# Optimization experiments

Measured on AMD Instinct MI355X. Metric: run time of the kernel, lower is better.

## Reference

```python
import jax, jax.numpy as jnp
import numpy as np

NUM_ORI = 4
VM_R, VM_RG = 10.0, 15.0
B_INH, G_INH = 1.5, 1.0
VM_W, VM_W2 = 0.1, 0.4
VM_WG, VM_W2G = 0.2, 0.4
BORDER_K = 11   # int(10*1.1)=11, already odd
GROUP_K = 23    # int(15*1.5)=22 -> +1 to make odd


def create_von_mises(size, r0, theta0, centered, w, w2):
    x = np.arange(size) - size / 2
    y = -(np.arange(size) - size / 2)
    X, Y = np.meshgrid(x, y)
    if centered:
        X = X + r0 * np.cos(theta0)
        Y = Y + r0 * np.sin(theta0)
    r = np.sqrt(X ** 2 + Y ** 2)
    th = np.arctan2(Y, X)
    # np.i0 == scipy.special.iv(0, .) for real args (I0 is even)
    return np.exp(r0 * w * np.cos(th - theta0)) / np.i0(w2 * (r - r0))


def make_filters():
    borders, groups = [], []
    for ori in np.arange(0.0, 180.0, 180.0 / NUM_ORI):
        a = ori * np.pi / 180.0
        b = (ori + 180.0) * np.pi / 180.0
        borders.append(create_von_mises(BORDER_K, VM_R, a, True, VM_W, VM_W2))
        borders.append(create_von_mises(BORDER_K, VM_R, b, True, VM_W, VM_W2))
        g1 = create_von_mises(GROUP_K, VM_RG, a, False, VM_W, VM_W2)
        g2 = create_von_mises(GROUP_K, VM_RG, b, False, VM_WG, VM_W2G)
        groups += [g1, g1, g2, g2]
    # only border filters are normalized to [-1, 1] in the original code
    borders = [f / (f.max() / 2.0) - 1.0 for f in borders]
    Wb = np.stack(borders)[:, None].astype(np.float32)   # [2*O, 1, 11, 11]
    Wg = np.stack(groups)[:, None].astype(np.float32)    # [4*O, 1, 23, 23]
    return jnp.asarray(Wb), jnp.asarray(Wg)


def setup_inputs() -> dict:
    key = jax.random.key(0)
    inp = jax.random.uniform(key, (4, 2, 512, 512), dtype=jnp.float32)
    Wb, Wg = make_filters()
    return {"inp": inp, "W_border": Wb, "W_group": Wg}


def _conv(x, w, pad, groups):
    return jax.lax.conv_general_dilated(
        x, w, (1, 1), [(pad, pad), (pad, pad)],
        dimension_numbers=("NCHW", "OIHW", "NCHW"),
        feature_group_count=groups)


def _spike(v):
    # LIF with tau_mem=0.01, zero initial v_mem, single step: alpha=exp(-1/tau)~0,
    # so v_mem = input; spike when v_mem >= threshold (1.0).
    return (v >= 1.0).astype(v.dtype)


def reference(inp, W_border, W_group):
    B, _, H, W = inp.shape
    pad_b = (BORDER_K - 1) // 2
    pad_g = (GROUP_K - 1) // 2
    # border ownership: conv each polarity with the 8 von-Mises filters + LIF
    pos = _spike(_conv(inp[:, 0:1], W_border, pad_b, 1))  # [B, 2*O, H, W]
    neg = _spike(_conv(inp[:, 1:2], W_border, pad_b, 1))
    vmap_ = inp.sum(1)[:, None]                           # [B, 1, H, W]
    pe, po = pos[:, 0::2], pos[:, 1::2]   # even=ori, odd=opposite ori
    ne, no = neg[:, 0::2], neg[:, 1::2]
    b13 = _spike(vmap_ * (pe - no * B_INH)) + _spike(vmap_ * (ne - po * B_INH))
    b24 = _spike(vmap_ * (po - ne * B_INH)) + _spike(vmap_ * (no - pe * B_INH))
    # winner-take-all over orientations
    diff = b13 - b24                                      # [B, O, H, W]
    tp = jnp.abs(diff)
    wta = jax.lax.stop_gradient(
        (tp == tp.max(axis=1, keepdims=True)).astype(inp.dtype))
    b1p = _spike(wta * diff)
    b1n = _spike(-(wta * diff))
    # channel order is ori-major: [t1_o, t2_o, t3_o, t4_o] per orientation
    border = jnp.stack(
        [b1p * b13, b1p * b24 * G_INH, b1n * b24, b1n * b13 * G_INH],
        axis=2).reshape(B, 4 * NUM_ORI, H, W)
    g = _spike(_conv(border, W_group, pad_g, 4 * NUM_ORI))
    g = g.reshape(B, NUM_ORI, 4, H, W)
    return (_spike(g[:, :, 0] - g[:, :, 1])
            + _spike(g[:, :, 2] - g[:, :, 3])).sum(1)     # [B, H, W]
```

## Files before the change

kernel.cpp:

```cpp
#include <hip/hip_runtime.h>

#define HH 512
#define WW 512
#define NB 4

typedef float v2f __attribute__((ext_vector_type(2)));

#define K1 11
#define PAD1 5
#define T1X 32
#define T1Y 32
#define IN1 42
#define S1B 44

__global__ __launch_bounds__(256, 4) void stage1_kernel(
    const float* __restrict__ inp, const float* __restrict__ Wb,
    unsigned char* __restrict__ border)
{
    __shared__ __align__(16) float s0[IN1 * S1B];
    __shared__ __align__(16) float s1[IN1 * S1B];

    const int b   = blockIdx.z;
    const int tx0 = blockIdx.x * T1X;
    const int ty0 = blockIdx.y * T1Y;
    const float* in0 = inp + ((size_t)b * 2 + 0) * (HH * WW);
    const float* in1 = inp + ((size_t)b * 2 + 1) * (HH * WW);

    for (int i = threadIdx.x; i < IN1 * IN1; i += 256) {
        int iy = i / IN1, ix = i - iy * IN1;
        int gy = ty0 + iy - PAD1, gx = tx0 + ix - PAD1;
        bool ok = (gy >= 0) & (gy < HH) & (gx >= 0) & (gx < WW);
        int idx = gy * WW + gx;
        s0[iy * S1B + ix] = ok ? in0[idx] : 0.f;
        s1[iy * S1B + ix] = ok ? in1[idx] : 0.f;
    }
    __syncthreads();

    const int lx  = threadIdx.x & 7;
    const int ly  = threadIdx.x >> 3;
    const int px0 = lx * 4;
    const int py  = ly;

    float accP[8][4], accN[8][4];
    #pragma unroll
    for (int c = 0; c < 8; c++)
        #pragma unroll
        for (int p = 0; p < 4; p++) { accP[c][p] = 0.f; accN[c][p] = 0.f; }

    #pragma unroll 1
    for (int ky = 0; ky < K1; ky++) {
        float a0[14], a1[14];
        const float2* r0 = (const float2*)&s0[(py + ky) * S1B + px0];
        const float2* r1 = (const float2*)&s1[(py + ky) * S1B + px0];
        #pragma unroll
        for (int r = 0; r < 7; r++) {
            *(float2*)&a0[2 * r] = r0[r];
            *(float2*)&a1[2 * r] = r1[r];
        }
        #pragma unroll
        for (int c = 0; c < 8; c++) {
            #pragma unroll
            for (int kx = 0; kx < K1; kx++) {
                const float wv = Wb[c * 121 + ky * 11 + kx];
                #pragma unroll
                for (int p = 0; p < 4; p++) {
                    accP[c][p] = fmaf(a0[kx + p], wv, accP[c][p]);
                    accN[c][p] = fmaf(a1[kx + p], wv, accN[c][p]);
                }
            }
        }
    }

    const int gy  = ty0 + py;
    const int gxb = tx0 + px0;

    float vm[4];
    #pragma unroll
    for (int p = 0; p < 4; p++)
        vm[p] = s0[(py + PAD1) * S1B + px0 + PAD1 + p]
              + s1[(py + PAD1) * S1B + px0 + PAD1 + p];

    float b13[4][4], b24[4][4];
    #pragma unroll
    for (int o = 0; o < 4; o++) {
        #pragma unroll
        for (int p = 0; p < 4; p++) {
            float pe = (accP[2 * o    ][p] >= 1.f) ? 1.f : 0.f;
            float po = (accP[2 * o + 1][p] >= 1.f) ? 1.f : 0.f;
            float ne = (accN[2 * o    ][p] >= 1.f) ? 1.f : 0.f;
            float no = (accN[2 * o + 1][p] >= 1.f) ? 1.f : 0.f;
            float sa = (vm[p] * (pe - 1.5f * no) >= 1.f) ? 1.f : 0.f;
            float sb = (vm[p] * (ne - 1.5f * po) >= 1.f) ? 1.f : 0.f;
            b13[o][p] = sa + sb;
            float sc = (vm[p] * (po - 1.5f * ne) >= 1.f) ? 1.f : 0.f;
            float sd = (vm[p] * (no - 1.5f * pe) >= 1.f) ? 1.f : 0.f;
            b24[o][p] = sc + sd;
        }
    }
    float mxp[4];
    #pragma unroll
    for (int p = 0; p < 4; p++) {
        float m = 0.f;
        #pragma unroll
        for (int o = 0; o < 4; o++) m = fmaxf(m, fabsf(b13[o][p] - b24[o][p]));
        mxp[p] = m;
    }
    #pragma unroll
    for (int o = 0; o < 4; o++) {
        unsigned w0 = 0, w1 = 0, w2 = 0, w3 = 0;
        #pragma unroll
        for (int p = 0; p < 4; p++) {
            float d   = b13[o][p] - b24[o][p];
            float wta = (fabsf(d) == mxp[p]) ? 1.f : 0.f;
            float b1p = (wta * d >= 1.f)    ? 1.f : 0.f;
            float b1n = (-(wta * d) >= 1.f) ? 1.f : 0.f;
            w0 |= (unsigned)(unsigned char)(b1p * b13[o][p]) << (8 * p);
            w1 |= (unsigned)(unsigned char)(b1p * b24[o][p]) << (8 * p);
            w2 |= (unsigned)(unsigned char)(b1n * b24[o][p]) << (8 * p);
            w3 |= (unsigned)(unsigned char)(b1n * b13[o][p]) << (8 * p);
        }
        size_t base = (((size_t)b * 16 + 4 * o) * HH + gy) * WW + gxb;
        *(unsigned*)&border[base]                       = w0;
        *(unsigned*)&border[base + (size_t)HH * WW]     = w1;
        *(unsigned*)&border[base + (size_t)2 * HH * WW] = w2;
        *(unsigned*)&border[base + (size_t)3 * HH * WW] = w3;
    }
}

#define K2 23
#define PAD2 11
#define T2X 32
#define T2Y 256
#define SROW 18
#define R2 278

__device__ __forceinline__ float ubyte_f(unsigned dw, int byi) {
    return (float)((dw >> (8 * byi)) & 0xffu);
}

__device__ __forceinline__ void s2_load(const unsigned* __restrict__ tile,
                                        int trow, int lx, unsigned d[8])
{
    const uint2* tp2 = (const uint2*)&tile[trow * SROW + 2 * lx];
    #pragma unroll
    for (int r2 = 0; r2 < 4; r2++) {
        uint2 v = tp2[r2];
        d[2 * r2] = v.x; d[2 * r2 + 1] = v.y;
    }
}

__global__ __launch_bounds__(256, 4) void stage2_kernel(
    const unsigned char* __restrict__ border, const float* __restrict__ Wg,
    unsigned char* __restrict__ gsp)
{
    __shared__ unsigned tile[R2 * SROW];

    const int z   = blockIdx.z;
    const int b   = z >> 4;
    const int c   = z & 15;
    const int tx0 = blockIdx.x * T2X;
    const int ty0 = blockIdx.y * T2Y;
    const unsigned char* bp = border + ((size_t)b * 16 + c) * (HH * WW);

    for (int i = threadIdx.x; i < R2 * 16; i += 256) {
        int iy = i >> 4, cc = i & 15;
        int gy  = ty0 - PAD2 + iy;
        int gx0 = tx0 - 12 + 4 * cc;
        unsigned u = 0;
        if (((unsigned)gy < HH) & ((unsigned)gx0 < WW))
            u = *(const unsigned*)(bp + (size_t)gy * WW + gx0);
        tile[iy * SROW + cc] = u;
    }
    __syncthreads();

    const int lx = threadIdx.x & 3;
    const int ly = threadIdx.x >> 2;
    const int px = lx * 8;
    const int py = ly * 4;

    v2f acc2[4][4];
    #pragma unroll
    for (int dy = 0; dy < 4; dy++)
        #pragma unroll
        for (int i = 0; i < 4; i++) acc2[dy][i] = (v2f){0.f, 0.f};

    const float* wc = Wg + c * (K2 * K2);

    unsigned dc[8];
    s2_load(tile, py + 0, lx, dc);

    #pragma unroll 1
    for (int t = 0; t < 26; t++) {
        v2f aE[15], aO[15];
        #pragma unroll
        for (int e = 0; e < 15; e++)
            aE[e] = (v2f){ubyte_f(dc[(2*e)   >> 2], (2*e)   & 3),
                          ubyte_f(dc[(2*e+1) >> 2], (2*e+1) & 3)};
        #pragma unroll
        for (int o = 0; o < 15; o++)
            aO[o] = (v2f){ubyte_f(dc[(2*o+1) >> 2], (2*o+1) & 3),
                          ubyte_f(dc[(2*o+2) >> 2], (2*o+2) & 3)};
        if (t < 25) s2_load(tile, py + t + 1, lx, dc);

        #pragma unroll
        for (int dy = 0; dy < 4; dy++) {
            const int ky = t - dy;
            if (ky >= 0 && ky < K2) {
                const float* wr = wc + ky * K2;
                #pragma unroll
                for (int kx = 0; kx < K2; kx++) {
                    const float wv = wr[kx];
                    const v2f wb = (v2f){wv, wv};
                    #pragma unroll
                    for (int i = 0; i < 4; i++) {
                        const v2f op = (kx & 1) ? aE[i + (kx + 1) / 2]
                                                : aO[i + kx / 2];
                        acc2[dy][i] = __builtin_elementwise_fma(op, wb, acc2[dy][i]);
                    }
                }
            }
        }
    }

    const int ox = tx0 + px;
    unsigned char* gp = gsp + ((size_t)b * 16 + c) * (HH * WW);
    #pragma unroll
    for (int dy = 0; dy < 4; dy++) {
        const int oy = ty0 + py + dy;
        unsigned lo = 0, hi = 0;
        #pragma unroll
        for (int i = 0; i < 2; i++) {
            lo |= (acc2[dy][i].x >= 1.f ? 1u : 0u) << (16 * i);
            lo |= (acc2[dy][i].y >= 1.f ? 1u : 0u) << (16 * i + 8);
        }
        #pragma unroll
        for (int i = 0; i < 2; i++) {
            hi |= (acc2[dy][i + 2].x >= 1.f ? 1u : 0u) << (16 * i);
            hi |= (acc2[dy][i + 2].y >= 1.f ? 1u : 0u) << (16 * i + 8);
        }
        uint2 v; v.x = lo; v.y = hi;
        *(uint2*)&gp[(size_t)oy * WW + ox] = v;
    }
}

__global__ __launch_bounds__(256) void combine_kernel(
    const unsigned char* __restrict__ gsp, float* __restrict__ out)
{
    const int idx = blockIdx.x * 256 + threadIdx.x;
    const int b = idx >> 16;
    const int r = idx & 65535;
    const unsigned* g = (const unsigned*)gsp;
    const int pb = b * 16;
    unsigned s = 0;
    #pragma unroll
    for (int o = 0; o < 4; o++) {
        unsigned g0 = g[(size_t)(pb + 4 * o + 0) * 65536 + r];
        unsigned g1 = g[(size_t)(pb + 4 * o + 1) * 65536 + r];
        unsigned g2 = g[(size_t)(pb + 4 * o + 2) * 65536 + r];
        unsigned g3 = g[(size_t)(pb + 4 * o + 3) * 65536 + r];
        s += ((g0 & ~g1) & 0x01010101u) + ((g2 & ~g3) & 0x01010101u);
    }
    float4 f;
    f.x = (float)(s & 255u);
    f.y = (float)((s >> 8) & 255u);
    f.z = (float)((s >> 16) & 255u);
    f.w = (float)(s >> 24);
    ((float4*)out)[idx] = f;
}

extern "C" void kernel_launch(void* const* d_in, const int* in_sizes, int n_in,
                              void* d_out, int out_size, void* d_ws, size_t ws_size,
                              hipStream_t stream)
{
    const float* inp = (const float*)d_in[0];
    const float* Wb  = (const float*)d_in[1];
    const float* Wg  = (const float*)d_in[2];
    unsigned char* border = (unsigned char*)d_ws;
    unsigned char* gsp    = border + (size_t)NB * 16 * HH * WW;
    float* out = (float*)d_out;

    dim3 blk(256);
    dim3 g1(WW / T1X, HH / T1Y, NB);
    stage1_kernel<<<g1, blk, 0, stream>>>(inp, Wb, border);
    dim3 g2(WW / T2X, HH / T2Y, NB * 16);
    stage2_kernel<<<g2, blk, 0, stream>>>(border, Wg, gsp);
    dim3 g3((NB * HH * WW / 4) / 256);
    combine_kernel<<<g3, blk, 0, stream>>>(gsp, out);
}
```

Measured before the change: 277.1 us.

## Pair channels per block and reuse each converted input row across output rows

Each stage-2 block now processes a pair of group channels (A and B) and writes the pairwise spike difference directly, halving the grid and the combine kernel's reads. The tap loop is split into prologue, steady-state and epilogue phases. In the steady state each input row is converted once and applied to all four output rows with scalar FMAs, so there is less per-tap branching and fewer conversions. The cost is double the LDS tile and more accumulators (64 floats), which raises register pressure and may lower occupancy under the launch bounds.

```diff
diff --git a/kernel.cpp b/kernel.cpp
--- a/kernel.cpp
+++ b/kernel.cpp
@@ -3,8 +3,6 @@
 #define HH 512
 #define WW 512
 #define NB 4
-
-typedef float v2f __attribute__((ext_vector_type(2)));
 
 #define K1 11
 #define PAD1 5
@@ -149,27 +147,38 @@
     }
 }
 
+__device__ __forceinline__ void s2_cvt(const unsigned d[8], float a[31])
+{
+    #pragma unroll
+    for (int j = 1; j <= 30; j++) a[j] = ubyte_f(d[j >> 2], j & 3);
+}
+
 __global__ __launch_bounds__(256, 4) void stage2_kernel(
     const unsigned char* __restrict__ border, const float* __restrict__ Wg,
     unsigned char* __restrict__ gsp)
 {
-    __shared__ unsigned tile[R2 * SROW];
+    __shared__ unsigned tileA[R2 * SROW];
+    __shared__ unsigned tileB[R2 * SROW];
 
     const int z   = blockIdx.z;
-    const int b   = z >> 4;
-    const int c   = z & 15;
+    const int b   = z >> 3;
+    const int q   = z & 7;
     const int tx0 = blockIdx.x * T2X;
     const int ty0 = blockIdx.y * T2Y;
-    const unsigned char* bp = border + ((size_t)b * 16 + c) * (HH * WW);
+    const unsigned char* bpA = border + ((size_t)b * 16 + 2 * q)     * (HH * WW);
+    const unsigned char* bpB = border + ((size_t)b * 16 + 2 * q + 1) * (HH * WW);
 
     for (int i = threadIdx.x; i < R2 * 16; i += 256) {
         int iy = i >> 4, cc = i & 15;
         int gy  = ty0 - PAD2 + iy;
         int gx0 = tx0 - 12 + 4 * cc;
-        unsigned u = 0;
-        if (((unsigned)gy < HH) & ((unsigned)gx0 < WW))
-            u = *(const unsigned*)(bp + (size_t)gy * WW + gx0);
-        tile[iy * SROW + cc] = u;
+        unsigned uA = 0, uB = 0;
+        if (((unsigned)gy < HH) & ((unsigned)gx0 < WW)) {
+            uA = *(const unsigned*)(bpA + (size_t)gy * WW + gx0);
+            uB = *(const unsigned*)(bpB + (size_t)gy * WW + gx0);
+        }
+        tileA[iy * SROW + cc] = uA;
+        tileB[iy * SROW + cc] = uB;
     }
     __syncthreads();
 
@@ -178,65 +187,127 @@
     const int px = lx * 8;
     const int py = ly * 4;
 
-    v2f acc2[4][4];
+    float accA[4][8], accB[4][8];
     #pragma unroll
     for (int dy = 0; dy < 4; dy++)
         #pragma unroll
-        for (int i = 0; i < 4; i++) acc2[dy][i] = (v2f){0.f, 0.f};
-
-    const float* wc = Wg + c * (K2 * K2);
-
-    unsigned dc[8];
-    s2_load(tile, py + 0, lx, dc);
+        for (int p = 0; p < 8; p++) { accA[dy][p] = 0.f; accB[dy][p] = 0.f; }
+
+    const float* wcA = Wg + (2 * q)     * (K2 * K2);
+    const float* wcB = Wg + (2 * q + 1) * (K2 * K2);
+
+    unsigned dcA[8], dcB[8];
+    s2_load(tileA, py + 0, lx, dcA);
+    s2_load(tileB, py + 0, lx, dcB);
 
     #pragma unroll 1
-    for (int t = 0; t < 26; t++) {
-        v2f aE[15], aO[15];
-        #pragma unroll
-        for (int e = 0; e < 15; e++)
-            aE[e] = (v2f){ubyte_f(dc[(2*e)   >> 2], (2*e)   & 3),
-                          ubyte_f(dc[(2*e+1) >> 2], (2*e+1) & 3)};
-        #pragma unroll
-        for (int o = 0; o < 15; o++)
-            aO[o] = (v2f){ubyte_f(dc[(2*o+1) >> 2], (2*o+1) & 3),
-                          ubyte_f(dc[(2*o+2) >> 2], (2*o+2) & 3)};
-        if (t < 25) s2_load(tile, py + t + 1, lx, dc);
-
+    for (int t = 0; t < 3; t++) {
+        float aA[31], aB[31];
+        s2_cvt(dcA, aA); s2_cvt(dcB, aB);
+        s2_load(tileA, py + t + 1, lx, dcA);
+        s2_load(tileB, py + t + 1, lx, dcB);
         #pragma unroll
         for (int dy = 0; dy < 4; dy++) {
-            const int ky = t - dy;
-            if (ky >= 0 && ky < K2) {
-                const float* wr = wc + ky * K2;
+            if (t - dy >= 0) {
+                const float* wrA = wcA + (t - dy) * K2;
+                const float* wrB = wcB + (t - dy) * K2;
                 #pragma unroll
                 for (int kx = 0; kx < K2; kx++) {
-                    const float wv = wr[kx];
-                    const v2f wb = (v2f){wv, wv};
+                    const float wA = wrA[kx];
+                    const float wB = wrB[kx];
                     #pragma unroll
-                    for (int i = 0; i < 4; i++) {
-                        const v2f op = (kx & 1) ? aE[i + (kx + 1) / 2]
-                                                : aO[i + kx / 2];
-                        acc2[dy][i] = __builtin_elementwise_fma(op, wb, acc2[dy][i]);
+                    for (int p = 0; p < 8; p++) {
+                        accA[dy][p] = fmaf(aA[p + kx + 1], wA, accA[dy][p]);
+                        accB[dy][p] = fmaf(aB[p + kx + 1], wB, accB[dy][p]);
                     }
                 }
             }
         }
     }
 
+    #pragma unroll 1
+    for (int t = 3; t < 23; t++) {
+        float aA[31], aB[31];
+        s2_cvt(dcA, aA); s2_cvt(dcB, aB);
+        s2_load(tileA, py + t + 1, lx, dcA);
+        s2_load(tileB, py + t + 1, lx, dcB);
+        const float* wA0 = wcA + t * K2;
+        const float* wB0 = wcB + t * K2;
+        #pragma unroll
+        for (int kx = 0; kx < K2; kx++) {
+            float wvA[4], wvB[4];
+            #pragma unroll
+            for (int d = 0; d < 4; d++) { wvA[d] = wA0[kx - 23 * d];
+                                          wvB[d] = wB0[kx - 23 * d]; }
+            #pragma unroll
+            for (int p = 0; p < 8; p++) {
+                const float avA = aA[p + kx + 1];
+                const float avB = aB[p + kx + 1];
+                #pragma unroll
+                for (int d = 0; d < 4; d++) {
+                    accA[d][p] = fmaf(avA, wvA[d], accA[d][p]);
+                    accB[d][p] = fmaf(avB, wvB[d], accB[d][p]);
+                }
+            }
+        }
+    }
+
+    #pragma unroll 1
+    for (int t = 23; t < 25; t++) {
+        float aA[31], aB[31];
+        s2_cvt(dcA, aA); s2_cvt(dcB, aB);
+        s2_load(tileA, py + t + 1, lx, dcA);
+        s2_load(tileB, py + t + 1, lx, dcB);
+        #pragma unroll
+        for (int dy = 0; dy < 4; dy++) {
+            if (t - dy < K2) {
+                const float* wrA = wcA + (t - dy) * K2;
+                const float* wrB = wcB + (t - dy) * K2;
+                #pragma unroll
+                for (int kx = 0; kx < K2; kx++) {
+                    const float wA = wrA[kx];
+                    const float wB = wrB[kx];
+                    #pragma unroll
+                    for (int p = 0; p < 8; p++) {
+                        accA[dy][p] = fmaf(aA[p + kx + 1], wA, accA[dy][p]);
+                        accB[dy][p] = fmaf(aB[p + kx + 1], wB, accB[dy][p]);
+                    }
+                }
+            }
+        }
+    }
+    {
+        float aA[31], aB[31];
+        s2_cvt(dcA, aA); s2_cvt(dcB, aB);
+        const float* wrA = wcA + 22 * K2;
+        const float* wrB = wcB + 22 * K2;
+        #pragma unroll
+        for (int kx = 0; kx < K2; kx++) {
+            const float wA = wrA[kx];
+            const float wB = wrB[kx];
+            #pragma unroll
+            for (int p = 0; p < 8; p++) {
+                accA[3][p] = fmaf(aA[p + kx + 1], wA, accA[3][p]);
+                accB[3][p] = fmaf(aB[p + kx + 1], wB, accB[3][p]);
+            }
+        }
+    }
+
     const int ox = tx0 + px;
-    unsigned char* gp = gsp + ((size_t)b * 16 + c) * (HH * WW);
+    unsigned char* gp = gsp + ((size_t)b * 8 + q) * (HH * WW);
     #pragma unroll
     for (int dy = 0; dy < 4; dy++) {
         const int oy = ty0 + py + dy;
         unsigned lo = 0, hi = 0;
         #pragma unroll
-        for (int i = 0; i < 2; i++) {
-            lo |= (acc2[dy][i].x >= 1.f ? 1u : 0u) << (16 * i);
-            lo |= (acc2[dy][i].y >= 1.f ? 1u : 0u) << (16 * i + 8);
-        }
-        #pragma unroll
-        for (int i = 0; i < 2; i++) {
-            hi |= (acc2[dy][i + 2].x >= 1.f ? 1u : 0u) << (16 * i);
-            hi |= (acc2[dy][i + 2].y >= 1.f ? 1u : 0u) << (16 * i + 8);
+        for (int p = 0; p < 4; p++) {
+            unsigned v = ((accA[dy][p] >= 1.f) & (accB[dy][p] < 1.f)) ? 1u : 0u;
+            lo |= v << (8 * p);
+        }
+        #pragma unroll
+        for (int p = 0; p < 4; p++) {
+            unsigned v = ((accA[dy][p + 4] >= 1.f) & (accB[dy][p + 4] < 1.f)) ? 1u : 0u;
+            hi |= v << (8 * p);
         }
         uint2 v; v.x = lo; v.y = hi;
         *(uint2*)&gp[(size_t)oy * WW + ox] = v;
@@ -250,16 +321,11 @@
     const int b = idx >> 16;
     const int r = idx & 65535;
     const unsigned* g = (const unsigned*)gsp;
-    const int pb = b * 16;
+    const int pb = b * 8;
     unsigned s = 0;
     #pragma unroll
-    for (int o = 0; o < 4; o++) {
-        unsigned g0 = g[(size_t)(pb + 4 * o + 0) * 65536 + r];
-        unsigned g1 = g[(size_t)(pb + 4 * o + 1) * 65536 + r];
-        unsigned g2 = g[(size_t)(pb + 4 * o + 2) * 65536 + r];
-        unsigned g3 = g[(size_t)(pb + 4 * o + 3) * 65536 + r];
-        s += ((g0 & ~g1) & 0x01010101u) + ((g2 & ~g3) & 0x01010101u);
-    }
+    for (int qq = 0; qq < 8; qq++)
+        s += g[(size_t)(pb + qq) * 65536 + r];
     float4 f;
     f.x = (float)(s & 255u);
     f.y = (float)((s >> 8) & 255u);
@@ -282,7 +348,7 @@
     dim3 blk(256);
     dim3 g1(WW / T1X, HH / T1Y, NB);
     stage1_kernel<<<g1, blk, 0, stream>>>(inp, Wb, border);
-    dim3 g2(WW / T2X, HH / T2Y, NB * 16);
+    dim3 g2(WW / T2X, HH / T2Y, NB * 8);
     stage2_kernel<<<g2, blk, 0, stream>>>(border, Wg, gsp);
     dim3 g3((NB * HH * WW / 4) / 256);
     combine_kernel<<<g3, blk, 0, stream>>>(gsp, out);
```

Result: slower. 435.3 us (+57.1%).
